# Optimization experiments

Measured on AMD Instinct MI355X. Metric: run time of the kernel, lower is better.

## Reference

```python
import jax, jax.numpy as jnp
import numpy as np

N_OBJ, IN_DIM, MID_DIM, OUT_DIM = 2048, 128, 256, 1


def setup_inputs() -> dict:
    key = jax.random.key(0)
    ks = jax.random.split(key, 7)
    s = 0.05  # keep sigmoid inputs in a sane range
    return {
        "x": jax.random.normal(ks[0], (N_OBJ, IN_DIM), dtype=jnp.float32),
        "W1": jax.random.normal(ks[1], (N_OBJ, MID_DIM, IN_DIM), dtype=jnp.float32) * s,
        "b1": jax.random.normal(ks[2], (N_OBJ, MID_DIM), dtype=jnp.float32) * s,
        "W2": jax.random.normal(ks[3], (N_OBJ, MID_DIM, MID_DIM), dtype=jnp.float32) * s,
        "b2": jax.random.normal(ks[4], (N_OBJ, MID_DIM), dtype=jnp.float32) * s,
        "W3": jax.random.normal(ks[5], (N_OBJ, OUT_DIM, MID_DIM), dtype=jnp.float32) * s,
        "b3": jax.random.normal(ks[6], (N_OBJ, OUT_DIM), dtype=jnp.float32) * s,
    }


def reference(x, W1, b1, W2, b2, W3, b3):
    # Per-object 3-layer MLP, batched as grouped GEMV over the object axis.
    # NOTE: faithful to original — NO activation after fc1.
    y1 = jnp.einsum("oi,omi->om", x, W1) + b1            # [O, mid]
    y2 = jax.nn.sigmoid(jnp.einsum("om,onm->on", y1, W2) + b2)  # [O, mid]
    y3 = jax.nn.sigmoid(jnp.einsum("on,okn->ok", y2, W3) + b3)  # [O, 1]
    return y3[:, 0]  # [n_objects]
```

## Files before the change

kernel.cpp:

```cpp
#include <hip/hip_runtime.h>
#include <math.h>


#define N_OBJ   2048
#define IN_DIM  128
#define MID_DIM 256

__global__ __launch_bounds__(256, 8) void mlp_grouped_kernel(
    const float* __restrict__ x,
    const float* __restrict__ W1,
    const float* __restrict__ b1,
    const float* __restrict__ W2,
    const float* __restrict__ b2,
    const float* __restrict__ W3,
    const float* __restrict__ b3,
    float* __restrict__ out)
{
    const int o = blockIdx.x;
    const int t = threadIdx.x;
    const int w = t >> 6;
    const int l = t & 63;

    __shared__ __align__(16) float s_y1[MID_DIM];
    __shared__ __align__(16) float s_y2[MID_DIM];

    {
        const int sub = l & 31;
        const int rh  = l >> 5;
        const float4 xv = *(const float4*)(x + (size_t)o * IN_DIM + sub * 4);
        const float* W1o = W1 + (size_t)o * MID_DIM * IN_DIM;

        #pragma unroll 4
        for (int i = 0; i < 32; ++i) {
            const int row = w * 64 + 2 * i + rh;
            float4 wv = *(const float4*)(W1o + (size_t)row * IN_DIM + sub * 4);
            float acc = wv.x * xv.x + wv.y * xv.y + wv.z * xv.z + wv.w * xv.w;
            acc += __shfl_xor(acc, 16, 32);
            acc += __shfl_xor(acc,  8, 32);
            acc += __shfl_xor(acc,  4, 32);
            acc += __shfl_xor(acc,  2, 32);
            acc += __shfl_xor(acc,  1, 32);
            if (sub == 0)
                s_y1[row] = acc + b1[(size_t)o * MID_DIM + row];
        }
    }
    __syncthreads();

    {
        const float4 yv = *(const float4*)(s_y1 + l * 4);
        const float* W2o = W2 + (size_t)o * MID_DIM * MID_DIM;

        #pragma unroll 4
        for (int i = 0; i < 64; ++i) {
            const int row = w * 64 + i;
            float4 wv = *(const float4*)(W2o + (size_t)row * MID_DIM + l * 4);
            float acc = wv.x * yv.x + wv.y * yv.y + wv.z * yv.z + wv.w * yv.w;
            acc += __shfl_xor(acc, 32, 64);
            acc += __shfl_xor(acc, 16, 64);
            acc += __shfl_xor(acc,  8, 64);
            acc += __shfl_xor(acc,  4, 64);
            acc += __shfl_xor(acc,  2, 64);
            acc += __shfl_xor(acc,  1, 64);
            if (l == 0) {
                float z = acc + b2[(size_t)o * MID_DIM + row];
                s_y2[row] = 1.0f / (1.0f + expf(-z));
            }
        }
    }
    __syncthreads();

    if (w == 0) {
        const float4 yv = *(const float4*)(s_y2 + l * 4);
        const float4 wv = *(const float4*)(W3 + (size_t)o * MID_DIM + l * 4);
        float acc = wv.x * yv.x + wv.y * yv.y + wv.z * yv.z + wv.w * yv.w;
        acc += __shfl_xor(acc, 32, 64);
        acc += __shfl_xor(acc, 16, 64);
        acc += __shfl_xor(acc,  8, 64);
        acc += __shfl_xor(acc,  4, 64);
        acc += __shfl_xor(acc,  2, 64);
        acc += __shfl_xor(acc,  1, 64);
        if (l == 0) {
            float z = acc + b3[o];
            out[o] = 1.0f / (1.0f + expf(-z));
        }
    }
}

extern "C" void kernel_launch(void* const* d_in, const int* in_sizes, int n_in,
                              void* d_out, int out_size, void* d_ws, size_t ws_size,
                              hipStream_t stream) {
    const float* x  = (const float*)d_in[0];
    const float* W1 = (const float*)d_in[1];
    const float* b1 = (const float*)d_in[2];
    const float* W2 = (const float*)d_in[3];
    const float* b2 = (const float*)d_in[4];
    const float* W3 = (const float*)d_in[5];
    const float* b3 = (const float*)d_in[6];
    float* out = (float*)d_out;

    mlp_grouped_kernel<<<N_OBJ, 256, 0, stream>>>(x, W1, b1, W2, b2, W3, b3, out);
}
```

Before: 835.6 us.

## Software-pipeline weight loads with nontemporal prefetch registers and stage biases in LDS

Replaces the simple unrolled weight loops with explicit register prefetch pipelines: W1 rows are loaded 4 ahead and W2 rows 8 ahead using nontemporal loads. The first W2 batch and the W3 vector are issued before the preceding barriers so their latency overlaps the sync and the prior layer. Biases b1 and b2 are staged into shared memory up front, and launch bounds drop to 4 waves per EU to leave registers for the prefetch buffers. The aim is more memory-level parallelism on this bandwidth-bound grouped GEMV. The cost is higher register pressure and potentially lower occupancy.

```diff
diff --git a/kernel.cpp b/kernel.cpp
--- a/kernel.cpp
+++ b/kernel.cpp
@@ -6,7 +6,9 @@
 #define IN_DIM  128
 #define MID_DIM 256
 
-__global__ __launch_bounds__(256, 8) void mlp_grouped_kernel(
+using f4 = __attribute__((ext_vector_type(4))) float;
+
+__global__ __launch_bounds__(256, 4) void mlp_grouped_kernel(
     const float* __restrict__ x,
     const float* __restrict__ W1,
     const float* __restrict__ b1,
@@ -23,56 +25,99 @@
 
     __shared__ __align__(16) float s_y1[MID_DIM];
     __shared__ __align__(16) float s_y2[MID_DIM];
+    __shared__ float s_b1[MID_DIM];
+    __shared__ float s_b2[MID_DIM];
+
+    s_b1[t] = b1[(size_t)o * MID_DIM + t];
+    s_b2[t] = b2[(size_t)o * MID_DIM + t];
 
     {
         const int sub = l & 31;
         const int rh  = l >> 5;
-        const float4 xv = *(const float4*)(x + (size_t)o * IN_DIM + sub * 4);
+        const f4 xv = *(const f4*)(x + (size_t)o * IN_DIM + sub * 4);
         const float* W1o = W1 + (size_t)o * MID_DIM * IN_DIM;
 
-        #pragma unroll 4
-        for (int i = 0; i < 32; ++i) {
-            const int row = w * 64 + 2 * i + rh;
-            float4 wv = *(const float4*)(W1o + (size_t)row * IN_DIM + sub * 4);
-            float acc = wv.x * xv.x + wv.y * xv.y + wv.z * xv.z + wv.w * xv.w;
-            acc += __shfl_xor(acc, 16, 32);
-            acc += __shfl_xor(acc,  8, 32);
-            acc += __shfl_xor(acc,  4, 32);
-            acc += __shfl_xor(acc,  2, 32);
-            acc += __shfl_xor(acc,  1, 32);
-            if (sub == 0)
-                s_y1[row] = acc + b1[(size_t)o * MID_DIM + row];
+        f4 pf[4];
+        #pragma unroll
+        for (int k = 0; k < 4; ++k) {
+            const int row = w * 64 + 2 * k + rh;
+            pf[k] = __builtin_nontemporal_load(
+                (const f4*)(W1o + (size_t)row * IN_DIM) + sub);
+        }
+
+        for (int ii = 0; ii < 8; ++ii) {
+            #pragma unroll
+            for (int k = 0; k < 4; ++k) {
+                f4 wv = pf[k];
+                const int ni = (ii + 1) * 4 + k;
+                if (ni < 32) {
+                    const int nrow = w * 64 + 2 * ni + rh;
+                    pf[k] = __builtin_nontemporal_load(
+                        (const f4*)(W1o + (size_t)nrow * IN_DIM) + sub);
+                }
+                const int i = ii * 4 + k;
+                const int row = w * 64 + 2 * i + rh;
+                float acc = wv[0] * xv[0] + wv[1] * xv[1]
+                          + wv[2] * xv[2] + wv[3] * xv[3];
+                acc += __shfl_xor(acc, 16, 32);
+                acc += __shfl_xor(acc,  8, 32);
+                acc += __shfl_xor(acc,  4, 32);
+                acc += __shfl_xor(acc,  2, 32);
+                acc += __shfl_xor(acc,  1, 32);
+                if (sub == 0)
+                    s_y1[row] = acc + s_b1[row];
+            }
         }
     }
+
+    const float* W2o = W2 + (size_t)o * MID_DIM * MID_DIM;
+    f4 pf2[8];
+    #pragma unroll
+    for (int k = 0; k < 8; ++k)
+        pf2[k] = __builtin_nontemporal_load(
+            (const f4*)(W2o + (size_t)(w * 64 + k) * MID_DIM) + l);
+
     __syncthreads();
 
     {
-        const float4 yv = *(const float4*)(s_y1 + l * 4);
-        const float* W2o = W2 + (size_t)o * MID_DIM * MID_DIM;
+        const f4 yv = *(const f4*)(s_y1 + l * 4);
 
-        #pragma unroll 4
-        for (int i = 0; i < 64; ++i) {
-            const int row = w * 64 + i;
-            float4 wv = *(const float4*)(W2o + (size_t)row * MID_DIM + l * 4);
-            float acc = wv.x * yv.x + wv.y * yv.y + wv.z * yv.z + wv.w * yv.w;
-            acc += __shfl_xor(acc, 32, 64);
-            acc += __shfl_xor(acc, 16, 64);
-            acc += __shfl_xor(acc,  8, 64);
-            acc += __shfl_xor(acc,  4, 64);
-            acc += __shfl_xor(acc,  2, 64);
-            acc += __shfl_xor(acc,  1, 64);
-            if (l == 0) {
-                float z = acc + b2[(size_t)o * MID_DIM + row];
-                s_y2[row] = 1.0f / (1.0f + expf(-z));
+        for (int ii = 0; ii < 8; ++ii) {
+            #pragma unroll
+            for (int k = 0; k < 8; ++k) {
+                f4 wv = pf2[k];
+                const int ni = (ii + 1) * 8 + k;
+                if (ni < 64) {
+                    pf2[k] = __builtin_nontemporal_load(
+                        (const f4*)(W2o + (size_t)(w * 64 + ni) * MID_DIM) + l);
+                }
+                const int row = w * 64 + ii * 8 + k;
+                float acc = wv[0] * yv[0] + wv[1] * yv[1]
+                          + wv[2] * yv[2] + wv[3] * yv[3];
+                acc += __shfl_xor(acc, 32, 64);
+                acc += __shfl_xor(acc, 16, 64);
+                acc += __shfl_xor(acc,  8, 64);
+                acc += __shfl_xor(acc,  4, 64);
+                acc += __shfl_xor(acc,  2, 64);
+                acc += __shfl_xor(acc,  1, 64);
+                if (l == 0) {
+                    float z = acc + s_b2[row];
+                    s_y2[row] = 1.0f / (1.0f + expf(-z));
+                }
             }
         }
     }
+
+    f4 w3v;
+    if (w == 0)
+        w3v = __builtin_nontemporal_load((const f4*)(W3 + (size_t)o * MID_DIM) + l);
+
     __syncthreads();
 
     if (w == 0) {
-        const float4 yv = *(const float4*)(s_y2 + l * 4);
-        const float4 wv = *(const float4*)(W3 + (size_t)o * MID_DIM + l * 4);
-        float acc = wv.x * yv.x + wv.y * yv.y + wv.z * yv.z + wv.w * yv.w;
+        const f4 yv = *(const f4*)(s_y2 + l * 4);
+        float acc = w3v[0] * yv[0] + w3v[1] * yv[1]
+                  + w3v[2] * yv[2] + w3v[3] * yv[3];
         acc += __shfl_xor(acc, 32, 64);
         acc += __shfl_xor(acc, 16, 64);
         acc += __shfl_xor(acc,  8, 64);
```

After: 802.7 us. 1.04x faster.
